# Optimization experiments

Hardware: AMD Instinct MI355X
Metric: run time of the kernel (lower is better)

The kernel has to match this reference:

```python
import jax, jax.numpy as jnp
import numpy as np

B, N, F_IN, F_OUT = 8, 8192, 128, 128
EPS = 1e-12  # F.normalize default eps


def setup_inputs() -> dict:
    key = jax.random.key(0)
    k1, k2, k3, k4 = jax.random.split(key, 4)
    x = jax.random.normal(k1, (B, N, F_IN), dtype=jnp.float32)
    adj = jax.random.uniform(k2, (N, N), dtype=jnp.float32)
    weight = jax.random.normal(k3, (F_IN, F_OUT), dtype=jnp.float32) * 0.05
    bias = jax.random.normal(k4, (F_OUT,), dtype=jnp.float32) * 0.05
    return {"x": x, "adj": adj, "weight": weight, "bias": bias}


def reference(x, adj, weight, bias):
    # Aggregate: equivalent to torch.sparse.mm(adj, x^T.reshape(N, B*F)) then
    # un-reshape/transpose — i.e. y[b] = adj @ x[b] for every batch element.
    y = jnp.einsum('nm,bmf->bnf', adj, x)  # [B, N, F_in]
    y = y + x                               # add_self
    y = jnp.einsum('bnf,fo->bno', y, weight) + bias  # dense transform + bias
    # L2 normalize along feature dim (F.normalize, p=2, dim=2)
    norm = jnp.sqrt(jnp.sum(y * y, axis=2, keepdims=True))
    y = y / jnp.maximum(norm, EPS)
    return y
```

## Files before the change

kernel.cpp:

```cpp
#include <hip/hip_runtime.h>
#include <hip/hip_bf16.h>
#include <stdint.h>


typedef __bf16 bf16;
typedef __bf16 bf16x8 __attribute__((ext_vector_type(8)));
typedef float floatx4 __attribute__((ext_vector_type(4)));

#define B_ 8
#define N_ 8192
#define F_ 128

__device__ __forceinline__ void async_copy16(const void* g, void* l) {
  __builtin_amdgcn_global_load_lds(
      (const __attribute__((address_space(1))) uint32_t*)g,
      (__attribute__((address_space(3))) uint32_t*)l, 16, 0, 0);
}

__global__ __launch_bounds__(256) void k0a_xw(const float* __restrict__ x,
                                              const float* __restrict__ w,
                                              bf16* __restrict__ u) {
  const int t = blockIdx.x * 256 + threadIdx.x;
  const int o0 = (t & 15) << 3;
  const size_t bm = (size_t)(t >> 4);
  const float* xr = x + bm * F_;
  float acc[8] = {};
  for (int f0 = 0; f0 < 128; f0 += 4) {
    float4 xv = *(const float4*)(xr + f0);
#pragma unroll
    for (int ff = 0; ff < 4; ++ff) {
      const float* wr_ = w + (size_t)(f0 + ff) * F_ + o0;
      float4 w0 = *(const float4*)(wr_);
      float4 w1 = *(const float4*)(wr_ + 4);
      float xf = (&xv.x)[ff];
      acc[0] += xf * w0.x; acc[1] += xf * w0.y;
      acc[2] += xf * w0.z; acc[3] += xf * w0.w;
      acc[4] += xf * w1.x; acc[5] += xf * w1.y;
      acc[6] += xf * w1.z; acc[7] += xf * w1.w;
    }
  }
  bf16x8 res;
#pragma unroll
  for (int jj = 0; jj < 8; ++jj) res[jj] = (bf16)acc[jj];
  *(bf16x8*)(u + bm * F_ + o0) = res;
}

__global__ __launch_bounds__(256) void k0b_transpose(const bf16* __restrict__ u,
                                                     bf16* __restrict__ ut) {
  __shared__ bf16 T[64][65];
  const int b = blockIdx.z;
  const int m0 = blockIdx.x << 6;
  const int o0 = blockIdx.y << 6;
  const bf16* up = u + (size_t)b * N_ * F_;
  bf16* utp = ut + (size_t)b * F_ * N_;
#pragma unroll
  for (int c = 0; c < 16; ++c) {
    int idx = threadIdx.x + (c << 8);
    int r = idx >> 6, cc = idx & 63;
    T[r][cc] = up[(size_t)(m0 + r) * F_ + o0 + cc];
  }
  __syncthreads();
#pragma unroll
  for (int c = 0; c < 16; ++c) {
    int idx = threadIdx.x + (c << 8);
    int r = idx >> 6, cc = idx & 63;
    utp[(size_t)(o0 + r) * N_ + m0 + cc] = T[cc][r];
  }
}

__global__ __launch_bounds__(512, 4) void k1_graphconv(const float* __restrict__ adj,
                                                       const bf16* __restrict__ ut,
                                                       const bf16* __restrict__ unat,
                                                       const float* __restrict__ bias,
                                                       float* __restrict__ out) {
  __shared__ bf16 As[128][64];
  __shared__ bf16 Bs[128][64];
  __shared__ float ss[2][128];
  const int tid = threadIdx.x;
  const int lane = tid & 63;
  const int wv = tid >> 6;
  const int wr = wv >> 1;
  const int wc = wv & 1;
  const int n0 = blockIdx.x << 7;
  const int b = blockIdx.y;
  const bf16* ub = ut + (size_t)b * F_ * N_;

  const int brow = tid >> 3;
  const int blc = (tid & 7) ^ (brow & 7);
  const bf16* gb0 = ub + (size_t)brow * N_ + (blc << 3);
  const bf16* gb1 = ub + (size_t)(brow + 64) * N_ + (blc << 3);
  bf16* lb0 = (bf16*)Bs + tid * 8;
  bf16* lb1 = (bf16*)Bs + (tid + 512) * 8;

  const int ar = tid >> 2;
  const int kc = (tid & 3) << 4;
  const float* gAb = adj + (size_t)(n0 + ar) * N_ + kc;
  const int pc0 = ((tid & 3) << 1) ^ (ar & 7);
  bf16* lA0 = (bf16*)As + ar * 64 + (pc0 << 3);
  bf16* lA1 = (bf16*)As + ar * 64 + ((pc0 ^ 1) << 3);

  const bf16* pa[2][2];
  const bf16* pb[4][2];
#pragma unroll
  for (int i = 0; i < 2; ++i)
#pragma unroll
    for (int kk = 0; kk < 2; ++kk)
      pa[i][kk] = &As[32 * wr + 16 * i + (lane & 15)]
                     [(((kk << 2) + (lane >> 4)) ^ (lane & 7)) << 3];
#pragma unroll
  for (int j = 0; j < 4; ++j)
#pragma unroll
    for (int kk = 0; kk < 2; ++kk)
      pb[j][kk] = &Bs[64 * wc + 16 * j + (lane & 15)]
                     [(((kk << 2) + (lane >> 4)) ^ (lane & 7)) << 3];

  floatx4 acc[2][4] = {};

  float4 pf[4];
#pragma unroll
  for (int q = 0; q < 4; ++q) pf[q] = *(const float4*)(gAb + 4 * q);

  for (int ks = 0; ks < 128; ++ks) {
    __syncthreads();
    async_copy16(gb0, lb0);
    async_copy16(gb1, lb1);
    gb0 += 64; gb1 += 64;
    bf16x8 lo, hi;
#pragma unroll
    for (int q = 0; q < 2; ++q) {
      float4 f = pf[q];
      lo[4 * q + 0] = (bf16)f.x; lo[4 * q + 1] = (bf16)f.y;
      lo[4 * q + 2] = (bf16)f.z; lo[4 * q + 3] = (bf16)f.w;
    }
#pragma unroll
    for (int q = 0; q < 2; ++q) {
      float4 f = pf[q + 2];
      hi[4 * q + 0] = (bf16)f.x; hi[4 * q + 1] = (bf16)f.y;
      hi[4 * q + 2] = (bf16)f.z; hi[4 * q + 3] = (bf16)f.w;
    }
    *(bf16x8*)lA0 = lo;
    *(bf16x8*)lA1 = hi;
    __syncthreads();
    const float* gn = gAb + ((size_t)((ks + 1) & 127) << 6);
#pragma unroll
    for (int q = 0; q < 4; ++q) pf[q] = *(const float4*)(gn + 4 * q);

#pragma unroll
    for (int kk = 0; kk < 2; ++kk) {
      bf16x8 av[2], bv[4];
#pragma unroll
      for (int i = 0; i < 2; ++i) av[i] = *(const bf16x8*)pa[i][kk];
#pragma unroll
      for (int j = 0; j < 4; ++j) bv[j] = *(const bf16x8*)pb[j][kk];
#pragma unroll
      for (int i = 0; i < 2; ++i)
#pragma unroll
        for (int j = 0; j < 4; ++j)
          acc[i][j] = __builtin_amdgcn_mfma_f32_16x16x32_bf16(av[i], bv[j],
                                                              acc[i][j], 0, 0, 0);
    }
  }

  float bo[4];
#pragma unroll
  for (int j = 0; j < 4; ++j) bo[j] = bias[64 * wc + 16 * j + (lane & 15)];

  const bf16* urow = unat + ((size_t)b * N_ + n0) * F_;

  float s[2][4];
#pragma unroll
  for (int i = 0; i < 2; ++i)
#pragma unroll
    for (int r = 0; r < 4; ++r) s[i][r] = 0.0f;
#pragma unroll
  for (int i = 0; i < 2; ++i)
#pragma unroll
    for (int j = 0; j < 4; ++j) {
      floatx4 t = acc[i][j];
      const int col = 64 * wc + 16 * j + (lane & 15);
#pragma unroll
      for (int r = 0; r < 4; ++r) {
        const int rowloc = 32 * wr + 16 * i + ((lane >> 4) << 2) + r;
        t[r] += bo[j] + (float)urow[(size_t)rowloc * F_ + col];
        s[i][r] += t[r] * t[r];
      }
      acc[i][j] = t;
    }
#pragma unroll
  for (int m = 1; m < 16; m <<= 1)
#pragma unroll
    for (int i = 0; i < 2; ++i)
#pragma unroll
      for (int r = 0; r < 4; ++r) s[i][r] += __shfl_xor(s[i][r], m, 16);

  if ((lane & 15) == 0) {
#pragma unroll
    for (int i = 0; i < 2; ++i)
#pragma unroll
      for (int r = 0; r < 4; ++r)
        ss[wc][32 * wr + 16 * i + ((lane >> 4) << 2) + r] = s[i][r];
  }
  __syncthreads();

  const size_t outbase = ((size_t)b * N_ + n0) * F_;
#pragma unroll
  for (int i = 0; i < 2; ++i)
#pragma unroll
    for (int r = 0; r < 4; ++r) {
      int rowloc = 32 * wr + 16 * i + ((lane >> 4) << 2) + r;
      float tot = ss[0][rowloc] + ss[1][rowloc];
      float inv = 1.0f / fmaxf(sqrtf(tot), 1e-12f);
      size_t ro = outbase + (size_t)rowloc * F_ + 64 * wc + (lane & 15);
#pragma unroll
      for (int j = 0; j < 4; ++j)
        out[ro + 16 * j] = acc[i][j][r] * inv;
    }
}

extern "C" void kernel_launch(void* const* d_in, const int* in_sizes, int n_in,
                              void* d_out, int out_size, void* d_ws, size_t ws_size,
                              hipStream_t stream) {
  (void)in_sizes; (void)n_in; (void)out_size; (void)ws_size;
  const float* x    = (const float*)d_in[0];
  const float* adj  = (const float*)d_in[1];
  const float* w    = (const float*)d_in[2];
  const float* bias = (const float*)d_in[3];
  float* out = (float*)d_out;
  bf16* u  = (bf16*)d_ws;
  bf16* ut = u + (size_t)B_ * N_ * F_;

  k0a_xw<<<dim3(4096), dim3(256), 0, stream>>>(x, w, u);
  k0b_transpose<<<dim3(128, 2, 8), dim3(256), 0, stream>>>(u, ut);
  k1_graphconv<<<dim3(64, 8), dim3(512), 0, stream>>>(adj, ut, u, bias, out);
}
```

Before: 669.3 us.

## Fuse x@W and transpose into one MFMA kernel writing transposed output

Replaces the scalar FP32 x@W kernel and the separate transpose kernel with one kernel. It stages x and W as bf16 in swizzled LDS, computes the product with MFMA, and writes the result directly in transposed layout. The graphconv epilogue now reads the self term from the transposed buffer, so the natural-layout copy is gone. This saves a launch, a full round trip of the intermediate, and slow scalar FMA work. The costs are that x is now rounded to bf16 before the matmul, and the epilogue reads the self term with a strided access pattern.

```diff
diff --git a/kernel.cpp b/kernel.cpp
--- a/kernel.cpp
+++ b/kernel.cpp
@@ -4,6 +4,7 @@
 
 
 typedef __bf16 bf16;
+typedef __bf16 bf16x4 __attribute__((ext_vector_type(4)));
 typedef __bf16 bf16x8 __attribute__((ext_vector_type(8)));
 typedef float floatx4 __attribute__((ext_vector_type(4)));
 
@@ -17,60 +18,94 @@
       (__attribute__((address_space(3))) uint32_t*)l, 16, 0, 0);
 }
 
-__global__ __launch_bounds__(256) void k0a_xw(const float* __restrict__ x,
-                                              const float* __restrict__ w,
-                                              bf16* __restrict__ u) {
-  const int t = blockIdx.x * 256 + threadIdx.x;
-  const int o0 = (t & 15) << 3;
-  const size_t bm = (size_t)(t >> 4);
-  const float* xr = x + bm * F_;
-  float acc[8] = {};
-  for (int f0 = 0; f0 < 128; f0 += 4) {
-    float4 xv = *(const float4*)(xr + f0);
-#pragma unroll
-    for (int ff = 0; ff < 4; ++ff) {
-      const float* wr_ = w + (size_t)(f0 + ff) * F_ + o0;
-      float4 w0 = *(const float4*)(wr_);
-      float4 w1 = *(const float4*)(wr_ + 4);
-      float xf = (&xv.x)[ff];
-      acc[0] += xf * w0.x; acc[1] += xf * w0.y;
-      acc[2] += xf * w0.z; acc[3] += xf * w0.w;
-      acc[4] += xf * w1.x; acc[5] += xf * w1.y;
-      acc[6] += xf * w1.z; acc[7] += xf * w1.w;
-    }
-  }
-  bf16x8 res;
-#pragma unroll
-  for (int jj = 0; jj < 8; ++jj) res[jj] = (bf16)acc[jj];
-  *(bf16x8*)(u + bm * F_ + o0) = res;
-}
-
-__global__ __launch_bounds__(256) void k0b_transpose(const bf16* __restrict__ u,
-                                                     bf16* __restrict__ ut) {
-  __shared__ bf16 T[64][65];
-  const int b = blockIdx.z;
-  const int m0 = blockIdx.x << 6;
-  const int o0 = blockIdx.y << 6;
-  const bf16* up = u + (size_t)b * N_ * F_;
-  bf16* utp = ut + (size_t)b * F_ * N_;
-#pragma unroll
-  for (int c = 0; c < 16; ++c) {
-    int idx = threadIdx.x + (c << 8);
-    int r = idx >> 6, cc = idx & 63;
-    T[r][cc] = up[(size_t)(m0 + r) * F_ + o0 + cc];
+__global__ __launch_bounds__(256, 2) void k0_xw_t(const float* __restrict__ x,
+                                                  const float* __restrict__ w,
+                                                  bf16* __restrict__ ut) {
+  __shared__ bf16 As[128][128];
+  __shared__ bf16 Wt[128][128];
+  const int tid = threadIdx.x;
+  const int lane = tid & 63;
+  const int l15 = lane & 15;
+  const int h = lane >> 4;
+  const int wv = tid >> 6;
+  const int wr = wv >> 1;
+  const int wc = wv & 1;
+  const int bm0 = blockIdx.x << 7;
+  const int b = bm0 >> 13;
+  const int m0 = bm0 & (N_ - 1);
+
+#pragma unroll
+  for (int c = 0; c < 64; ++c) {
+    int lin = (c << 8) + tid;
+    int f = lin >> 7, o = lin & 127;
+    bf16 v = (bf16)w[(size_t)f * F_ + o];
+    int phys = (f >> 3) ^ (o & 15);
+    ((bf16*)Wt)[o * 128 + (phys << 3) + (f & 7)] = v;
+  }
+
+  {
+    const int r = tid >> 1;
+    const int colh = (tid & 1) << 6;
+    const float* xr = x + (size_t)(bm0 + r) * F_ + colh;
+#pragma unroll
+    for (int q = 0; q < 8; ++q) {
+      float4 f0 = *(const float4*)(xr + 8 * q);
+      float4 f1 = *(const float4*)(xr + 8 * q + 4);
+      bf16x8 pk;
+      pk[0] = (bf16)f0.x; pk[1] = (bf16)f0.y; pk[2] = (bf16)f0.z; pk[3] = (bf16)f0.w;
+      pk[4] = (bf16)f1.x; pk[5] = (bf16)f1.y; pk[6] = (bf16)f1.z; pk[7] = (bf16)f1.w;
+      int c = ((tid & 1) << 3) + q;
+      int phys = c ^ (r & 15);
+      *(bf16x8*)&((bf16*)As)[r * 128 + (phys << 3)] = pk;
+    }
   }
   __syncthreads();
-#pragma unroll
-  for (int c = 0; c < 16; ++c) {
-    int idx = threadIdx.x + (c << 8);
-    int r = idx >> 6, cc = idx & 63;
-    utp[(size_t)(o0 + r) * N_ + m0 + cc] = T[cc][r];
-  }
+
+  const bf16* pa[4][4];
+  const bf16* pb[4][4];
+#pragma unroll
+  for (int i = 0; i < 4; ++i)
+#pragma unroll
+    for (int kk = 0; kk < 4; ++kk)
+      pa[i][kk] = &As[64 * wr + 16 * i + l15][(((kk << 2) + h) ^ l15) << 3];
+#pragma unroll
+  for (int j = 0; j < 4; ++j)
+#pragma unroll
+    for (int kk = 0; kk < 4; ++kk)
+      pb[j][kk] = &Wt[64 * wc + 16 * j + l15][(((kk << 2) + h) ^ l15) << 3];
+
+  floatx4 acc[4][4] = {};
+#pragma unroll
+  for (int kk = 0; kk < 4; ++kk) {
+    bf16x8 av[4], bv[4];
+#pragma unroll
+    for (int i = 0; i < 4; ++i) av[i] = *(const bf16x8*)pa[i][kk];
+#pragma unroll
+    for (int j = 0; j < 4; ++j) bv[j] = *(const bf16x8*)pb[j][kk];
+#pragma unroll
+    for (int i = 0; i < 4; ++i)
+#pragma unroll
+      for (int j = 0; j < 4; ++j)
+        acc[i][j] = __builtin_amdgcn_mfma_f32_16x16x32_bf16(av[i], bv[j],
+                                                            acc[i][j], 0, 0, 0);
+  }
+
+  bf16* utb = ut + (size_t)b * F_ * N_;
+#pragma unroll
+  for (int i = 0; i < 4; ++i)
+#pragma unroll
+    for (int j = 0; j < 4; ++j) {
+      const int o = 64 * wc + 16 * j + l15;
+      const int mrow = m0 + 64 * wr + 16 * i + (h << 2);
+      bf16x4 pk;
+#pragma unroll
+      for (int r = 0; r < 4; ++r) pk[r] = (bf16)acc[i][j][r];
+      *(bf16x4*)(utb + (size_t)o * N_ + mrow) = pk;
+    }
 }
 
 __global__ __launch_bounds__(512, 4) void k1_graphconv(const float* __restrict__ adj,
                                                        const bf16* __restrict__ ut,
-                                                       const bf16* __restrict__ unat,
                                                        const float* __restrict__ bias,
                                                        float* __restrict__ out) {
   __shared__ bf16 As[128][64];
@@ -165,8 +200,6 @@
 #pragma unroll
   for (int j = 0; j < 4; ++j) bo[j] = bias[64 * wc + 16 * j + (lane & 15)];
 
-  const bf16* urow = unat + ((size_t)b * N_ + n0) * F_;
-
   float s[2][4];
 #pragma unroll
   for (int i = 0; i < 2; ++i)
@@ -181,7 +214,7 @@
 #pragma unroll
       for (int r = 0; r < 4; ++r) {
         const int rowloc = 32 * wr + 16 * i + ((lane >> 4) << 2) + r;
-        t[r] += bo[j] + (float)urow[(size_t)rowloc * F_ + col];
+        t[r] += bo[j] + (float)ub[(size_t)col * N_ + n0 + rowloc];
         s[i][r] += t[r] * t[r];
       }
       acc[i][j] = t;
@@ -226,10 +259,8 @@
   const float* w    = (const float*)d_in[2];
   const float* bias = (const float*)d_in[3];
   float* out = (float*)d_out;
-  bf16* u  = (bf16*)d_ws;
-  bf16* ut = u + (size_t)B_ * N_ * F_;
-
-  k0a_xw<<<dim3(4096), dim3(256), 0, stream>>>(x, w, u);
-  k0b_transpose<<<dim3(128, 2, 8), dim3(256), 0, stream>>>(u, ut);
-  k1_graphconv<<<dim3(64, 8), dim3(512), 0, stream>>>(adj, ut, u, bias, out);
-}
+  bf16* ut = (bf16*)d_ws;
+
+  k0_xw_t<<<dim3(512), dim3(256), 0, stream>>>(x, w, ut);
+  k1_graphconv<<<dim3(64, 8), dim3(512), 0, stream>>>(adj, ut, bias, out);
+}
```

Measured after the change: 543.3 us. 1.23x faster.
